# Kernel optimization log

Measured on AMD Instinct MI355X. Metric: run time of the kernel, lower is better.

The kernel has to match this reference:

```python
import jax, jax.numpy as jnp
import numpy as np

DIM = 768
NUM_HEADS = 12
HEAD_DIM = DIM // NUM_HEADS


def setup_inputs() -> dict:
    key = jax.random.key(0)
    k1, k2, k3 = jax.random.split(key, 3)
    B, N = 2, 2048
    x = jax.random.normal(k1, (B, N, DIM), dtype=jnp.float32)
    qkv_w = jax.random.normal(k2, (3 * DIM, DIM), dtype=jnp.float32) * 0.02
    proj_w = jax.random.normal(k3, (DIM, DIM), dtype=jnp.float32) * 0.02
    proj_b = jnp.zeros((DIM,), dtype=jnp.float32)
    freq_params = jnp.ones((NUM_HEADS, 1), dtype=jnp.float32) * 0.5  # Parameter init ones*0.5
    return {"x": x, "qkv_w": qkv_w, "proj_w": proj_w, "proj_b": proj_b,
            "freq_params": freq_params}


def _forward(x, qkv_w, proj_w, proj_b, freq_params):
    B, N, C = x.shape
    H, D = NUM_HEADS, HEAD_DIM
    scale = D ** (-0.5)
    # qkv projection -> (3, B, H, N, D)
    qkv = (x @ qkv_w.T).reshape(B, N, 3, H, D).transpose(2, 0, 3, 1, 4)
    q, k, v = qkv[0], qkv[1], qkv[2]
    # FFT along the token axis (axis=2 of [B,H,N,D])
    q_freq = jnp.fft.fft(q, axis=2)
    k_freq = jnp.fft.fft(k, axis=2)
    # Adaptive per-head low-pass: cutoff = int(N * sigmoid(freq_param)),
    # frequencies >= cutoff attenuated by exp(-(i - cutoff) / (N/4)).
    cutoff = jnp.floor(N * jax.nn.sigmoid(freq_params[:, 0]))        # (H,)
    idx = jnp.arange(N, dtype=jnp.float32)                            # (N,)
    rel = idx[None, :] - cutoff[:, None]                              # (H, N)
    atten = jnp.where(rel >= 0, jnp.exp(-rel / (N / 4.0)), 1.0)       # (H, N)
    atten = atten[None, :, :, None]                                   # (1, H, N, 1)
    q_filt = jnp.fft.ifft(q_freq * atten, axis=2).real
    k_filt = jnp.fft.ifft(k_freq * atten, axis=2).real
    # Attention
    attn = jnp.einsum('bhnd,bhmd->bhnm', q_filt, k_filt) * scale
    attn = jax.nn.softmax(attn, axis=-1)
    out = jnp.einsum('bhnm,bhmd->bhnd', attn, v)
    out = out.transpose(0, 2, 1, 3).reshape(B, N, C)
    return out @ proj_w.T + proj_b


def reference(x, qkv_w, proj_w, proj_b, freq_params):
    return _forward(x, qkv_w, proj_w, proj_b, freq_params)
```

## Files before the change

kernel.cpp:

```cpp
#include <hip/hip_runtime.h>
#include <math.h>

#define SEQ 2048
#define NH 12
#define HD 64
#define DIM 768

typedef _Float16 half_t;
typedef _Float16 f16x8 __attribute__((ext_vector_type(8)));
typedef _Float16 f16x4 __attribute__((ext_vector_type(4)));
typedef float f32x4 __attribute__((ext_vector_type(4)));

__device__ __forceinline__ void dma16(const half_t* g, half_t* l) {
  __builtin_amdgcn_global_load_lds(
      (const __attribute__((address_space(1))) unsigned int*)g,
      (__attribute__((address_space(3))) unsigned int*)l, 16, 0, 0);
}

__global__ __launch_bounds__(256) void cvt_f32_f16(
    const float* __restrict__ a, const float* __restrict__ b,
    const float* __restrict__ c, half_t* __restrict__ a16,
    half_t* __restrict__ b16, half_t* __restrict__ c16) {
  const size_t NA = 786432, NB = 442368;
  size_t i = (size_t)blockIdx.x * 256 + threadIdx.x;
  if (i < NA + NB) {
    const float* src = (i < NA) ? a : b;
    half_t* dst = (i < NA) ? a16 : b16;
    size_t off = (i < NA) ? i : i - NA;
    float4 v = *(const float4*)&src[off * 4];
    f16x4 h;
    h[0] = (half_t)v.x; h[1] = (half_t)v.y; h[2] = (half_t)v.z; h[3] = (half_t)v.w;
    int row = (int)((off * 4) / DIM);
    int col = (int)((off * 4) % DIM);
    int sc = col ^ ((row & 7) << 3);
    *(f16x4*)&dst[(size_t)row * DIM + sc] = h;
  } else {
    size_t off = i - NA - NB;
    float4 v = *(const float4*)&c[off * 4];
    f16x4 h;
    h[0] = (half_t)v.x; h[1] = (half_t)v.y; h[2] = (half_t)v.z; h[3] = (half_t)v.w;
    *(f16x4*)&c16[off * 4] = h;
  }
}

__global__ __launch_bounds__(256) void gemm_qkv_f16(
    const half_t* __restrict__ xs, const half_t* __restrict__ ws,
    float* __restrict__ qT, float* __restrict__ kT, half_t* __restrict__ vb) {
  __shared__ half_t As[2][128][64];
  __shared__ half_t Bs[2][128][64];
  const int tid = threadIdx.x;
  const int lane = tid & 63, wave = tid >> 6;
  const int quad = lane >> 4, l16 = lane & 15;
  const int wr = wave >> 1, wc = wave & 1;
  const int row0 = blockIdx.y * 128;
  const int col0 = blockIdx.x * 128;
  const int rl = lane >> 3, ch = lane & 7;

#pragma unroll
  for (int i = 0; i < 4; i++) {
    int ins = wave * 4 + i;
    dma16(xs + (size_t)(row0 + ins * 8 + rl) * DIM + ch * 8, &As[0][ins * 8][0]);
    dma16(ws + (size_t)(col0 + ins * 8 + rl) * DIM + ch * 8, &Bs[0][ins * 8][0]);
  }

  f32x4 acc[4][4] = {};

  for (int c = 0; c < 12; c++) {
    const int cur = c & 1;
    __syncthreads();
    if (c < 11) {
      int k0 = (c + 1) * 64;
#pragma unroll
      for (int i = 0; i < 4; i++) {
        int ins = wave * 4 + i;
        dma16(xs + (size_t)(row0 + ins * 8 + rl) * DIM + k0 + ch * 8,
              &As[1 - cur][ins * 8][0]);
        dma16(ws + (size_t)(col0 + ins * 8 + rl) * DIM + k0 + ch * 8,
              &Bs[1 - cur][ins * 8][0]);
      }
    }
#pragma unroll
    for (int ks = 0; ks < 2; ks++) {
      f16x8 af[4], bf[4];
#pragma unroll
      for (int i = 0; i < 4; i++) {
        int rr = wr * 64 + i * 16 + l16;
        af[i] = *(const f16x8*)&As[cur][rr][((ks * 4 + quad) ^ (rr & 7)) << 3];
      }
#pragma unroll
      for (int j = 0; j < 4; j++) {
        int rr = wc * 64 + j * 16 + l16;
        bf[j] = *(const f16x8*)&Bs[cur][rr][((ks * 4 + quad) ^ (rr & 7)) << 3];
      }
#pragma unroll
      for (int i = 0; i < 4; i++)
#pragma unroll
        for (int j = 0; j < 4; j++)
          acc[i][j] = __builtin_amdgcn_mfma_f32_16x16x32_f16(af[i], bf[j], acc[i][j], 0, 0, 0);
    }
  }

  const int fbase = col0 + wc * 64;
#pragma unroll
  for (int i = 0; i < 4; i++) {
    int n = row0 + wr * 64 + i * 16 + quad * 4;
    int b = n >> 11, nn = n & (SEQ - 1);
#pragma unroll
    for (int j = 0; j < 4; j++) {
      int f = fbase + j * 16 + l16;
      if (col0 < 1536) {
        float* dst = (col0 < 768) ? qT : kT;
        int fo = (col0 < 768) ? f : f - 768;
        *(f32x4*)&dst[((size_t)(b * 768 + fo)) * SEQ + nn] = acc[i][j];
      } else {
        int fo = f - 1536;
        int h = fo >> 6, d = fo & 63;
        int bh = b * NH + h;
        int chn = nn >> 6, cw = (nn & 63) >> 3, sub = nn & 7;
        f16x4 hv;
#pragma unroll
        for (int r = 0; r < 4; r++) hv[r] = (half_t)acc[i][j][r];
        *(f16x4*)&vb[((((size_t)bh * 32 + chn) * 64 + d) << 6) +
                     (((cw ^ (d & 7)) << 3) + sub)] = hv;
      }
    }
  }
}

__device__ __forceinline__ void fft2048_dif_fwd(float* re, float* im, int tid) {
  for (int M = 2048; M >= 8; M >>= 2) {
    const int q = M >> 2;
    const float ang = -6.283185307179586f / (float)M;
#pragma unroll 2
    for (int g = tid; g < 512; g += 256) {
      int j = g & (q - 1);
      int base = ((g & ~(q - 1)) << 2) | j;
      float s1, c1;
      __sincosf(ang * (float)j, &s1, &c1);
      float c2 = c1 * c1 - s1 * s1, s2 = 2.0f * c1 * s1;
      float Ar = re[base],         Ai = im[base];
      float Br = re[base + q],     Bi = im[base + q];
      float Cr = re[base + 2*q],   Ci = im[base + 2*q];
      float Dr = re[base + 3*q],   Di = im[base + 3*q];
      float A1r = Ar + Cr, A1i = Ai + Ci;
      float t1r = Ar - Cr, t1i = Ai - Ci;
      float C1r = c1 * t1r - s1 * t1i, C1i = c1 * t1i + s1 * t1r;
      float B1r = Br + Dr, B1i = Bi + Di;
      float t2r = Br - Dr, t2i = Bi - Di;
      float u2r = c1 * t2r - s1 * t2i, u2i = c1 * t2i + s1 * t2r;
      float D1r = u2i, D1i = -u2r;
      re[base]         = A1r + B1r; im[base]         = A1i + B1i;
      float t3r = A1r - B1r, t3i = A1i - B1i;
      re[base + q]     = c2 * t3r - s2 * t3i;
      im[base + q]     = c2 * t3i + s2 * t3r;
      re[base + 2*q]   = C1r + D1r; im[base + 2*q]   = C1i + D1i;
      float t4r = C1r - D1r, t4i = C1i - D1i;
      re[base + 3*q]   = c2 * t4r - s2 * t4i;
      im[base + 3*q]   = c2 * t4i + s2 * t4r;
    }
    __syncthreads();
  }
#pragma unroll 2
  for (int i = tid; i < 1024; i += 256) {
    float ar = re[2*i], ai = im[2*i], br = re[2*i+1], bi = im[2*i+1];
    re[2*i]   = ar + br; im[2*i]   = ai + bi;
    re[2*i+1] = ar - br; im[2*i+1] = ai - bi;
  }
  __syncthreads();
}

__device__ __forceinline__ void fft2048_dit_inv(float* re, float* im, int tid) {
  for (int L = 2; L <= 512; L <<= 2) {
    const int h = L >> 1;
    const float ang = 3.14159265358979f / (float)L;
#pragma unroll 2
    for (int g = tid; g < SEQ / 4; g += 256) {
      int p = g & (h - 1);
      int i0 = ((g & ~(h - 1)) << 2) | p;
      float s2, c2;
      __sincosf(ang * (float)p, &s2, &c2);
      float c1 = c2 * c2 - s2 * s2, s1 = 2.0f * c2 * s2;
      float ar = re[i0],         ai = im[i0];
      float br = re[i0 + h],     bi = im[i0 + h];
      float cr = re[i0 + L],     ci = im[i0 + L];
      float dr = re[i0 + L + h], di = im[i0 + L + h];
      float t1r = c1 * br - s1 * bi, t1i = c1 * bi + s1 * br;
      float a1r = ar + t1r, a1i = ai + t1i;
      float b1r = ar - t1r, b1i = ai - t1i;
      float t2r = c1 * dr - s1 * di, t2i = c1 * di + s1 * dr;
      float e1r = cr + t2r, e1i = ci + t2i;
      float d1r = cr - t2r, d1i = ci - t2i;
      float ur = c2 * e1r - s2 * e1i, ui = c2 * e1i + s2 * e1r;
      float vr = c2 * d1r - s2 * d1i, vi = c2 * d1i + s2 * d1r;
      float wr = -vi, wi = vr;
      re[i0]         = a1r + ur; im[i0]         = a1i + ui;
      re[i0 + L]     = a1r - ur; im[i0 + L]     = a1i - ui;
      re[i0 + h]     = b1r + wr; im[i0 + h]     = b1i + wi;
      re[i0 + L + h] = b1r - wr; im[i0 + L + h] = b1i - wi;
    }
    __syncthreads();
  }
  {
    const float ang = 6.283185307179586f / 2048.0f;
#pragma unroll 2
    for (int j = tid; j < 1024; j += 256) {
      float s, c;
      __sincosf(ang * (float)j, &s, &c);
      float x0r = re[j], x0i = im[j], x1r = re[j + 1024], x1i = im[j + 1024];
      float tr = c * x1r - s * x1i, ti = c * x1i + s * x1r;
      re[j] = x0r + tr;        im[j] = x0i + ti;
      re[j + 1024] = x0r - tr; im[j + 1024] = x0i - ti;
    }
    __syncthreads();
  }
}

__global__ __launch_bounds__(256) void fft_filter(
    const float* __restrict__ qT, const float* __restrict__ kT,
    half_t* __restrict__ qh, half_t* __restrict__ kh,
    const float* __restrict__ freq_params) {
  __shared__ float re[SEQ];
  __shared__ float im[SEQ];
  const int tid = threadIdx.x;
  const int idx = blockIdx.x;
  const int h = (idx >> 6) % NH;
  const float* qrow = qT + (size_t)idx * SEQ;
  const float* krow = kT + (size_t)idx * SEQ;

  for (int n = tid; n < SEQ; n += 256) { re[n] = qrow[n]; im[n] = krow[n]; }
  __syncthreads();
  fft2048_dif_fwd(re, im, tid);

  const float fp = freq_params[h];
  const float sig = 1.0f / (1.0f + expf(-fp));
  const float cutoff = floorf((float)SEQ * sig);

#pragma unroll 2
  for (int p = tid; p < SEQ; p += 256) {
    int n = (int)(__brev((unsigned)p) >> 21);
    int m = (SEQ - n) & (SEQ - 1);
    float r1 = (float)n - cutoff;
    float r2 = (float)m - cutoff;
    float A1 = (r1 >= 0.0f) ? __expf(-r1 * (1.0f / 512.0f)) : 1.0f;
    float A2 = (r2 >= 0.0f) ? __expf(-r2 * (1.0f / 512.0f)) : 1.0f;
    float Ae = 0.5f * (A1 + A2);
    re[p] *= Ae; im[p] *= Ae;
  }
  __syncthreads();

  fft2048_dit_inv(re, im, tid);

  const float inv = 1.0f / (float)SEQ;
  half_t* qo = qh + (size_t)idx * SEQ;
  half_t* ko = kh + (size_t)idx * SEQ;
  for (int n = tid; n < SEQ; n += 256) {
    qo[n] = (half_t)(re[n] * inv);
    ko[n] = (half_t)(im[n] * inv);
  }
}

__global__ __launch_bounds__(256) void transpose_k16(
    const half_t* __restrict__ kh, half_t* __restrict__ kA) {
  __shared__ half_t tl[64][65];
  const int t = threadIdx.x;
  const int N0 = blockIdx.x * 64;
  const int bh = blockIdx.y;
#pragma unroll
  for (int i = 0; i < 2; i++) {
    int idx = i * 256 + t;
    int d = idx >> 3, n8 = (idx & 7) << 3;
    f16x8 v = *(const f16x8*)&kh[((size_t)(bh * 64 + d)) * SEQ + N0 + n8];
#pragma unroll
    for (int j = 0; j < 8; j++) tl[d][n8 + j] = v[j];
  }
  __syncthreads();
#pragma unroll
  for (int i = 0; i < 2; i++) {
    int idx = i * 256 + t;
    int nl = idx >> 3, chunk = idx & 7;
    f16x8 v;
#pragma unroll
    for (int j = 0; j < 8; j++) v[j] = tl[chunk * 8 + j][nl];
    *(f16x8*)&kA[((size_t)(bh * SEQ + N0 + nl)) * 64 + (chunk ^ (nl & 7)) * 8] = v;
  }
}

__global__ __launch_bounds__(256) void attention_v7(
    const half_t* __restrict__ q_h, const half_t* __restrict__ kA,
    const half_t* __restrict__ vb, float* __restrict__ part0,
    float* __restrict__ part1, float* __restrict__ Lp0,
    float* __restrict__ Lp1) {
  __shared__ half_t ks[2][64][64];
  __shared__ half_t vs[2][64][64];
  const int t = threadIdx.x;
  const int lane = t & 63, wave = t >> 6;
  const int quad = lane >> 4, l16 = lane & 15;
  const int id = blockIdx.x;
  const int bh = (id & 7) * 3 + ((id >> 3) % 3);
  const int rest = id / 24;
  const int qt = rest >> 1, mh = rest & 1;
  const int N0 = qt * 128;
  float* part = mh ? part1 : part0;
  float* Lp = mh ? Lp1 : Lp0;
  const half_t* kbase = kA + ((size_t)bh * SEQ + mh * 1024) * 64;
  const half_t* vbase = vb + (((size_t)bh * 32 + mh * 16) << 12);
  const half_t* qb = q_h + (size_t)bh * 64 * SEQ;

  f16x8 qlo[2], qhi[2];
#pragma unroll
  for (int u = 0; u < 2; u++) {
    int n = N0 + wave * 32 + u * 16 + l16;
#pragma unroll
    for (int e = 0; e < 8; e++) {
      qlo[u][e] = qb[(size_t)(quad * 8 + e) * SEQ + n];
      qhi[u][e] = qb[(size_t)(32 + quad * 8 + e) * SEQ + n];
    }
  }

#pragma unroll
  for (int i = 0; i < 2; i++) {
    int ins = wave * 2 + i;
    dma16(kbase + ins * 512 + lane * 8, &ks[0][ins * 8][0]);
    dma16(vbase + ins * 512 + lane * 8, &vs[0][ins * 8][0]);
  }

  f32x4 acc[2][4] = {};
  f32x4 accL[2] = {};
  f16x4 ones;
  ones[0] = (half_t)1.0f; ones[1] = (half_t)1.0f;
  ones[2] = (half_t)1.0f; ones[3] = (half_t)1.0f;
  const float SC = 0.18033688011112042f;
  const float SH = -2.8853900817779268f;

  for (int c = 0; c < 16; c++) {
    const int cur = c & 1;
    __syncthreads();

    const int cn = (c < 15) ? c + 1 : 0;
#pragma unroll
    for (int i = 0; i < 2; i++) {
      int ins = wave * 2 + i;
      dma16(kbase + (size_t)cn * 4096 + ins * 512 + lane * 8,
            &ks[1 - cur][ins * 8][0]);
      dma16(vbase + (size_t)cn * 4096 + ins * 512 + lane * 8,
            &vs[1 - cur][ins * 8][0]);
    }

    f16x4 pf[2][4];
#pragma unroll
    for (int j = 0; j < 4; j++) {
      int row = j * 16 + l16;
      int sw = row & 7;
      f16x8 klo = *(const f16x8*)&ks[cur][row][(quad ^ sw) * 8];
      f16x8 khi = *(const f16x8*)&ks[cur][row][((quad + 4) ^ sw) * 8];
#pragma unroll
      for (int u = 0; u < 2; u++) {
        f32x4 s = {};
        s = __builtin_amdgcn_mfma_f32_16x16x32_f16(klo, qlo[u], s, 0, 0, 0);
        s = __builtin_amdgcn_mfma_f32_16x16x32_f16(khi, qhi[u], s, 0, 0, 0);
#pragma unroll
        for (int r = 0; r < 4; r++)
          pf[u][j][r] = (half_t)exp2f(fmaf(s[r], SC, SH));
      }
    }

#pragma unroll
    for (int j = 0; j < 4; j++) {
      accL[0] = __builtin_amdgcn_mfma_f32_16x16x16f16(pf[0][j], ones, accL[0], 0, 0, 0);
      accL[1] = __builtin_amdgcn_mfma_f32_16x16x16f16(pf[1][j], ones, accL[1], 0, 0, 0);
#pragma unroll
      for (int dt = 0; dt < 4; dt++) {
        int d = dt * 16 + l16;
        int cc = ((2 * j + (quad >> 1)) ^ (d & 7));
        f16x4 bv = *(const f16x4*)&vs[cur][d][cc * 8 + (quad & 1) * 4];
        acc[0][dt] = __builtin_amdgcn_mfma_f32_16x16x16f16(pf[0][j], bv, acc[0][dt], 0, 0, 0);
        acc[1][dt] = __builtin_amdgcn_mfma_f32_16x16x16f16(pf[1][j], bv, acc[1][dt], 0, 0, 0);
      }
    }
  }

#pragma unroll
  for (int u = 0; u < 2; u++) {
    if (l16 == 0) {
#pragma unroll
      for (int r = 0; r < 4; r++)
        Lp[(size_t)bh * SEQ + N0 + wave * 32 + u * 16 + quad * 4 + r] = accL[u][r];
    }
#pragma unroll
    for (int dt = 0; dt < 4; dt++) {
#pragma unroll
      for (int r = 0; r < 4; r++) {
        int n = N0 + wave * 32 + u * 16 + quad * 4 + r;
        part[((size_t)bh * SEQ + n) * 64 + dt * 16 + l16] = acc[u][dt][r];
      }
    }
  }
}

__global__ __launch_bounds__(256) void combine_o(
    const float* __restrict__ p0, const float* __restrict__ p1,
    const float* __restrict__ L0, const float* __restrict__ L1,
    half_t* __restrict__ ao) {
  int idx = blockIdx.x * 256 + threadIdx.x;
  int row = idx >> 4;
  int d = (idx & 15) << 2;
  f32x4 a = *(const f32x4*)&p0[(size_t)row * 64 + d];
  f32x4 b = *(const f32x4*)&p1[(size_t)row * 64 + d];
  float inv = 1.0f / (L0[row] + L1[row]);
  int bh = row >> 11, n = row & (SEQ - 1);
  int bb = bh / NH, h = bh % NH;
  f16x4 o;
#pragma unroll
  for (int r = 0; r < 4; r++) o[r] = (half_t)((a[r] + b[r]) * inv);
  *(f16x4*)&ao[((size_t)(bb * SEQ + n)) * DIM + h * 64 + d] = o;
}

__global__ __launch_bounds__(256) void gemm_proj_f16(
    const half_t* __restrict__ ao, const half_t* __restrict__ w,
    const float* __restrict__ bias, float* __restrict__ out) {
  __shared__ half_t As[128][64];
  __shared__ half_t Bs[128][64];
  const int tid = threadIdx.x;
  const int lane = tid & 63, wave = tid >> 6;
  const int quad = lane >> 4, l16 = lane & 15;
  const int wr = wave >> 1, wc = wave & 1;
  const int row0 = blockIdx.y * 128;
  const int col0 = blockIdx.x * 128;
  const int srow = tid >> 3;
  const int schk = tid & 7;

  f32x4 acc[4][4] = {};

  for (int k0 = 0; k0 < DIM; k0 += 64) {
    f16x8 av[4], bv[4];
#pragma unroll
    for (int p = 0; p < 4; p++) {
      av[p] = *(const f16x8*)&ao[(size_t)(row0 + srow + p * 32) * DIM + k0 + schk * 8];
      bv[p] = *(const f16x8*)&w[(size_t)(col0 + srow + p * 32) * DIM + k0 + schk * 8];
    }
    __syncthreads();
#pragma unroll
    for (int p = 0; p < 4; p++) {
      int r = srow + p * 32;
      int cs = ((schk ^ (r & 7)) << 3);
      *(f16x8*)&As[r][cs] = av[p];
      *(f16x8*)&Bs[r][cs] = bv[p];
    }
    __syncthreads();
#pragma unroll
    for (int ks = 0; ks < 2; ks++) {
      f16x8 af[4], bf[4];
#pragma unroll
      for (int i = 0; i < 4; i++) {
        int rr = wr * 64 + i * 16 + l16;
        af[i] = *(const f16x8*)&As[rr][((ks * 4 + quad) ^ (rr & 7)) << 3];
      }
#pragma unroll
      for (int j = 0; j < 4; j++) {
        int rr = wc * 64 + j * 16 + l16;
        bf[j] = *(const f16x8*)&Bs[rr][((ks * 4 + quad) ^ (rr & 7)) << 3];
      }
#pragma unroll
      for (int i = 0; i < 4; i++)
#pragma unroll
        for (int j = 0; j < 4; j++)
          acc[i][j] = __builtin_amdgcn_mfma_f32_16x16x32_f16(af[i], bf[j], acc[i][j], 0, 0, 0);
    }
  }

#pragma unroll
  for (int i = 0; i < 4; i++) {
    int m = row0 + wr * 64 + i * 16 + quad * 4;
#pragma unroll
    for (int j = 0; j < 4; j++) {
      int f = col0 + wc * 64 + j * 16 + l16;
      float bj = bias[f];
#pragma unroll
      for (int r = 0; r < 4; r++)
        out[(size_t)(m + r) * DIM + f] = acc[i][j][r] + bj;
    }
  }
}

extern "C" void kernel_launch(void* const* d_in, const int* in_sizes, int n_in,
                              void* d_out, int out_size, void* d_ws, size_t ws_size,
                              hipStream_t stream) {
  (void)in_sizes; (void)n_in; (void)out_size; (void)ws_size;
  const float* x      = (const float*)d_in[0];
  const float* qkv_w  = (const float*)d_in[1];
  const float* proj_w = (const float*)d_in[2];
  const float* proj_b = (const float*)d_in[3];
  const float* freq   = (const float*)d_in[4];
  float* out = (float*)d_out;
  char* ws = (char*)d_ws;

  half_t* wp16 = (half_t*)(ws);
  float*  qT   = (float*)(ws + 1179648);
  float*  kT   = (float*)(ws + 13762560);
  half_t* v_b  = (half_t*)(ws + 26345472);
  half_t* x16  = (half_t*)(ws + 32636928);
  half_t* w16  = (half_t*)(ws + 38928384);
  half_t* q_h  = (half_t*)(ws + 42467328);
  half_t* k_h  = (half_t*)(ws + 32636928);
  float*  part0 = (float*)(ws + 1179648);
  float*  part1 = (float*)(ws + 13762560);
  float*  Lp0  = (float*)(ws + 38928384);
  float*  Lp1  = (float*)(ws + 38928384 + 196608);
  half_t* ao   = (half_t*)(ws + 42467328);
  half_t* kA   = (half_t*)d_out;

  cvt_f32_f16<<<5376, 256, 0, stream>>>(x, qkv_w, proj_w, x16, w16, wp16);
  gemm_qkv_f16<<<dim3(18, 32), 256, 0, stream>>>(x16, w16, qT, kT, v_b);
  fft_filter<<<1536, 256, 0, stream>>>(qT, kT, q_h, k_h, freq);
  transpose_k16<<<dim3(32, 24), 256, 0, stream>>>(k_h, kA);
  attention_v7<<<768, 256, 0, stream>>>(q_h, kA, v_b, part0, part1, Lp0, Lp1);
  combine_o<<<3072, 256, 0, stream>>>(part0, part1, Lp0, Lp1, ao);
  gemm_proj_f16<<<dim3(6, 32), 256, 0, stream>>>(ao, wp16, proj_b, out);
}
```

Before: 211.7 us.

## Fuse split-K combine into projection GEMM and halve attention query tile

```diff
diff --git a/kernel.cpp b/kernel.cpp
--- a/kernel.cpp
+++ b/kernel.cpp
@@ -232,7 +232,7 @@
   fft2048_dif_fwd(re, im, tid);
 
   const float fp = freq_params[h];
-  const float sig = 1.0f / (1.0f + expf(-fp));
+  const float sig = 1.0f / (1.0f + __expf(-fp));
   const float cutoff = floorf((float)SEQ * sig);
 
 #pragma unroll 2
@@ -250,11 +250,12 @@
 
   fft2048_dit_inv(re, im, tid);
 
+  const float invq = (1.0f / (float)SEQ) * 0.18033688011112042f;
   const float inv = 1.0f / (float)SEQ;
   half_t* qo = qh + (size_t)idx * SEQ;
   half_t* ko = kh + (size_t)idx * SEQ;
   for (int n = tid; n < SEQ; n += 256) {
-    qo[n] = (half_t)(re[n] * inv);
+    qo[n] = (half_t)(re[n] * invq);
     ko[n] = (half_t)(im[n] * inv);
   }
 }
@@ -285,7 +286,7 @@
   }
 }
 
-__global__ __launch_bounds__(256) void attention_v7(
+__global__ __launch_bounds__(256) void attention_v8(
     const half_t* __restrict__ q_h, const half_t* __restrict__ kA,
     const half_t* __restrict__ vb, float* __restrict__ part0,
     float* __restrict__ part1, float* __restrict__ Lp0,
@@ -299,21 +300,20 @@
   const int bh = (id & 7) * 3 + ((id >> 3) % 3);
   const int rest = id / 24;
   const int qt = rest >> 1, mh = rest & 1;
-  const int N0 = qt * 128;
+  const int N0 = qt * 64;
   float* part = mh ? part1 : part0;
   float* Lp = mh ? Lp1 : Lp0;
   const half_t* kbase = kA + ((size_t)bh * SEQ + mh * 1024) * 64;
   const half_t* vbase = vb + (((size_t)bh * 32 + mh * 16) << 12);
   const half_t* qb = q_h + (size_t)bh * 64 * SEQ;
 
-  f16x8 qlo[2], qhi[2];
-#pragma unroll
-  for (int u = 0; u < 2; u++) {
-    int n = N0 + wave * 32 + u * 16 + l16;
+  f16x8 qlo, qhi;
+  {
+    int n = N0 + wave * 16 + l16;
 #pragma unroll
     for (int e = 0; e < 8; e++) {
-      qlo[u][e] = qb[(size_t)(quad * 8 + e) * SEQ + n];
-      qhi[u][e] = qb[(size_t)(32 + quad * 8 + e) * SEQ + n];
+      qlo[e] = qb[(size_t)(quad * 8 + e) * SEQ + n];
+      qhi[e] = qb[(size_t)(32 + quad * 8 + e) * SEQ + n];
     }
   }
 
@@ -324,100 +324,81 @@
     dma16(vbase + ins * 512 + lane * 8, &vs[0][ins * 8][0]);
   }
 
-  f32x4 acc[2][4] = {};
-  f32x4 accL[2] = {};
+  f32x4 acc[4] = {};
+  f32x4 accL = {};
   f16x4 ones;
   ones[0] = (half_t)1.0f; ones[1] = (half_t)1.0f;
   ones[2] = (half_t)1.0f; ones[3] = (half_t)1.0f;
-  const float SC = 0.18033688011112042f;
-  const float SH = -2.8853900817779268f;
 
   for (int c = 0; c < 16; c++) {
     const int cur = c & 1;
     __syncthreads();
 
-    const int cn = (c < 15) ? c + 1 : 0;
-#pragma unroll
-    for (int i = 0; i < 2; i++) {
-      int ins = wave * 2 + i;
-      dma16(kbase + (size_t)cn * 4096 + ins * 512 + lane * 8,
-            &ks[1 - cur][ins * 8][0]);
-      dma16(vbase + (size_t)cn * 4096 + ins * 512 + lane * 8,
-            &vs[1 - cur][ins * 8][0]);
-    }
-
-    f16x4 pf[2][4];
+    if (c < 15) {
+      const int cn = c + 1;
+#pragma unroll
+      for (int i = 0; i < 2; i++) {
+        int ins = wave * 2 + i;
+        dma16(kbase + (size_t)cn * 4096 + ins * 512 + lane * 8,
+              &ks[1 - cur][ins * 8][0]);
+        dma16(vbase + (size_t)cn * 4096 + ins * 512 + lane * 8,
+              &vs[1 - cur][ins * 8][0]);
+      }
+    }
+
+    f16x4 pf[4];
 #pragma unroll
     for (int j = 0; j < 4; j++) {
       int row = j * 16 + l16;
       int sw = row & 7;
       f16x8 klo = *(const f16x8*)&ks[cur][row][(quad ^ sw) * 8];
       f16x8 khi = *(const f16x8*)&ks[cur][row][((quad + 4) ^ sw) * 8];
-#pragma unroll
-      for (int u = 0; u < 2; u++) {
-        f32x4 s = {};
-        s = __builtin_amdgcn_mfma_f32_16x16x32_f16(klo, qlo[u], s, 0, 0, 0);
-        s = __builtin_amdgcn_mfma_f32_16x16x32_f16(khi, qhi[u], s, 0, 0, 0);
-#pragma unroll
-        for (int r = 0; r < 4; r++)
-          pf[u][j][r] = (half_t)exp2f(fmaf(s[r], SC, SH));
-      }
+      f32x4 s = {};
+      s = __builtin_amdgcn_mfma_f32_16x16x32_f16(klo, qlo, s, 0, 0, 0);
+      s = __builtin_amdgcn_mfma_f32_16x16x32_f16(khi, qhi, s, 0, 0, 0);
+      float e0 = __builtin_amdgcn_exp2f(s[0]);
+      float e1 = __builtin_amdgcn_exp2f(s[1]);
+      float e2 = __builtin_amdgcn_exp2f(s[2]);
+      float e3 = __builtin_amdgcn_exp2f(s[3]);
+      auto plo = __builtin_amdgcn_cvt_pkrtz(e0, e1);
+      auto phi = __builtin_amdgcn_cvt_pkrtz(e2, e3);
+      pf[j][0] = (half_t)plo[0]; pf[j][1] = (half_t)plo[1];
+      pf[j][2] = (half_t)phi[0]; pf[j][3] = (half_t)phi[1];
     }
 
 #pragma unroll
     for (int j = 0; j < 4; j++) {
-      accL[0] = __builtin_amdgcn_mfma_f32_16x16x16f16(pf[0][j], ones, accL[0], 0, 0, 0);
-      accL[1] = __builtin_amdgcn_mfma_f32_16x16x16f16(pf[1][j], ones, accL[1], 0, 0, 0);
+      accL = __builtin_amdgcn_mfma_f32_16x16x16f16(pf[j], ones, accL, 0, 0, 0);
 #pragma unroll
       for (int dt = 0; dt < 4; dt++) {
         int d = dt * 16 + l16;
         int cc = ((2 * j + (quad >> 1)) ^ (d & 7));
         f16x4 bv = *(const f16x4*)&vs[cur][d][cc * 8 + (quad & 1) * 4];
-        acc[0][dt] = __builtin_amdgcn_mfma_f32_16x16x16f16(pf[0][j], bv, acc[0][dt], 0, 0, 0);
-        acc[1][dt] = __builtin_amdgcn_mfma_f32_16x16x16f16(pf[1][j], bv, acc[1][dt], 0, 0, 0);
-      }
-    }
-  }
-
-#pragma unroll
-  for (int u = 0; u < 2; u++) {
-    if (l16 == 0) {
-#pragma unroll
-      for (int r = 0; r < 4; r++)
-        Lp[(size_t)bh * SEQ + N0 + wave * 32 + u * 16 + quad * 4 + r] = accL[u][r];
-    }
-#pragma unroll
-    for (int dt = 0; dt < 4; dt++) {
-#pragma unroll
-      for (int r = 0; r < 4; r++) {
-        int n = N0 + wave * 32 + u * 16 + quad * 4 + r;
-        part[((size_t)bh * SEQ + n) * 64 + dt * 16 + l16] = acc[u][dt][r];
-      }
-    }
-  }
-}
-
-__global__ __launch_bounds__(256) void combine_o(
+        acc[dt] = __builtin_amdgcn_mfma_f32_16x16x16f16(pf[j], bv, acc[dt], 0, 0, 0);
+      }
+    }
+  }
+
+  if (l16 == 0) {
+#pragma unroll
+    for (int r = 0; r < 4; r++)
+      Lp[(size_t)bh * SEQ + N0 + wave * 16 + quad * 4 + r] = accL[r];
+  }
+#pragma unroll
+  for (int dt = 0; dt < 4; dt++) {
+#pragma unroll
+    for (int r = 0; r < 4; r++) {
+      int n = N0 + wave * 16 + quad * 4 + r;
+      part[((size_t)bh * SEQ + n) * 64 + dt * 16 + l16] = acc[dt][r];
+    }
+  }
+}
+
+__global__ __launch_bounds__(256) void gemm_proj_fused(
     const float* __restrict__ p0, const float* __restrict__ p1,
     const float* __restrict__ L0, const float* __restrict__ L1,
-    half_t* __restrict__ ao) {
-  int idx = blockIdx.x * 256 + threadIdx.x;
-  int row = idx >> 4;
-  int d = (idx & 15) << 2;
-  f32x4 a = *(const f32x4*)&p0[(size_t)row * 64 + d];
-  f32x4 b = *(const f32x4*)&p1[(size_t)row * 64 + d];
-  float inv = 1.0f / (L0[row] + L1[row]);
-  int bh = row >> 11, n = row & (SEQ - 1);
-  int bb = bh / NH, h = bh % NH;
-  f16x4 o;
-#pragma unroll
-  for (int r = 0; r < 4; r++) o[r] = (half_t)((a[r] + b[r]) * inv);
-  *(f16x4*)&ao[((size_t)(bb * SEQ + n)) * DIM + h * 64 + d] = o;
-}
-
-__global__ __launch_bounds__(256) void gemm_proj_f16(
-    const half_t* __restrict__ ao, const half_t* __restrict__ w,
-    const float* __restrict__ bias, float* __restrict__ out) {
+    const half_t* __restrict__ w, const float* __restrict__ bias,
+    float* __restrict__ out) {
   __shared__ half_t As[128][64];
   __shared__ half_t Bs[128][64];
   const int tid = threadIdx.x;
@@ -432,10 +413,26 @@
   f32x4 acc[4][4] = {};
 
   for (int k0 = 0; k0 < DIM; k0 += 64) {
-    f16x8 av[4], bv[4];
+    const int cbase = k0 + schk * 8;
+    const int h = cbase >> 6, d0 = cbase & 63;
+    f16x8 av[4];
+    f16x8 bv[4];
 #pragma unroll
     for (int p = 0; p < 4; p++) {
-      av[p] = *(const f16x8*)&ao[(size_t)(row0 + srow + p * 32) * DIM + k0 + schk * 8];
+      int mg = row0 + srow + p * 32;
+      int b = mg >> 11, nn = mg & (SEQ - 1);
+      size_t lrow = (size_t)(b * NH + h) * SEQ + nn;
+      size_t base = lrow * 64 + d0;
+      f32x4 a0 = *(const f32x4*)&p0[base];
+      f32x4 a1 = *(const f32x4*)&p0[base + 4];
+      f32x4 b0 = *(const f32x4*)&p1[base];
+      f32x4 b1 = *(const f32x4*)&p1[base + 4];
+      float invl = 1.0f / (L0[lrow] + L1[lrow]);
+#pragma unroll
+      for (int e = 0; e < 4; e++) {
+        av[p][e]     = (half_t)((a0[e] + b0[e]) * invl);
+        av[p][e + 4] = (half_t)((a1[e] + b1[e]) * invl);
+      }
       bv[p] = *(const f16x8*)&w[(size_t)(col0 + srow + p * 32) * DIM + k0 + schk * 8];
     }
     __syncthreads();
@@ -506,14 +503,12 @@
   float*  part1 = (float*)(ws + 13762560);
   float*  Lp0  = (float*)(ws + 38928384);
   float*  Lp1  = (float*)(ws + 38928384 + 196608);
-  half_t* ao   = (half_t*)(ws + 42467328);
   half_t* kA   = (half_t*)d_out;
 
   cvt_f32_f16<<<5376, 256, 0, stream>>>(x, qkv_w, proj_w, x16, w16, wp16);
   gemm_qkv_f16<<<dim3(18, 32), 256, 0, stream>>>(x16, w16, qT, kT, v_b);
   fft_filter<<<1536, 256, 0, stream>>>(qT, kT, q_h, k_h, freq);
   transpose_k16<<<dim3(32, 24), 256, 0, stream>>>(k_h, kA);
-  attention_v7<<<768, 256, 0, stream>>>(q_h, kA, v_b, part0, part1, Lp0, Lp1);
-  combine_o<<<3072, 256, 0, stream>>>(part0, part1, Lp0, Lp1, ao);
-  gemm_proj_f16<<<dim3(6, 32), 256, 0, stream>>>(ao, wp16, proj_b, out);
-}
+  attention_v8<<<1536, 256, 0, stream>>>(q_h, kA, v_b, part0, part1, Lp0, Lp1);
+  gemm_proj_fused<<<dim3(6, 32), 256, 0, stream>>>(part0, part1, Lp0, Lp1, wp16, proj_b, out);
+}
```

Result: no change. 213.3 us (+0.8%).
